# Kernel optimization log

Measured on AMD Instinct MI355X. Metric: run time of the kernel, lower is better.

## Reference

```python
import jax, jax.numpy as jnp
import numpy as np

B, V, M, C = 1024, 2, 256, 256  # batch, num_vars (must be 2), latent states, categories


def setup_inputs() -> dict:
    key = jax.random.key(0)
    k1, k2, k3 = jax.random.split(key, 3)
    x = jax.random.randint(k1, (B, V), 0, C)
    # input-node tables: per var v, per latent node k, a [M, C] row-normalized table
    W = jax.nn.softmax(jax.random.normal(k2, (V, M, M, C), dtype=jnp.float32), axis=-1)
    # sum-node mixture weights over the M product children
    w_sum = jax.nn.softmax(jax.random.normal(k3, (M,), dtype=jnp.float32))
    return {"x": x, "W": W, "w_sum": w_sum}


def reference(x, W, w_sum):
    # lp[v] has shape [M(k), M(m), B]: log W[v, k, m, x[b, v]]
    # (matches torch: probs[:, x_var].log() per input node, stacked over latent k)
    lp0 = jnp.log(W[0][:, :, x[:, 0]])  # [M, M, B]
    lp1 = jnp.log(W[1][:, :, x[:, 1]])  # [M, M, B]
    prod = lp0 + lp1                    # product nodes, [M(k), M, B]
    # sum node: log( sum_k w_k * exp(prod_k) ) -> [M, B]
    mixed = jnp.log(jnp.einsum('k,kmb->mb', w_sum, jnp.exp(prod)))
    # root: logsumexp over the leading M dim -> [B]
    return jax.nn.logsumexp(mixed, axis=0)
```

## Files before the change

kernel.cpp:

```cpp
#include <hip/hip_runtime.h>
#include <math.h>


#define SPLITS  256
#define KCHUNK  256
#define BK      32
#define NITER   (KCHUNK / BK)
#define LDSS    40

typedef float  f32x4  __attribute__((ext_vector_type(4)));
typedef short  bf16x8 __attribute__((ext_vector_type(8)));

static __device__ __forceinline__ short f2bf(float f) {
    unsigned u = __builtin_bit_cast(unsigned, f);
    u += 0x7fffu + ((u >> 16) & 1u);
    return (short)(u >> 16);
}

__global__ __launch_bounds__(512, 2) void hclt_fused_kernel(
    const int* __restrict__ x, const float* __restrict__ W,
    const float* __restrict__ wsum, float* __restrict__ S_b,
    int* __restrict__ counter, float* __restrict__ out)
{
    __shared__ __align__(16) char smem[81920];
    __shared__ int pairs[1024];
    __shared__ int lastFlag;

    short* const AsB[2] = { (short*)smem,           (short*)(smem + 20480) };
    short* const BsB[2] = { (short*)(smem + 40960), (short*)(smem + 61440) };
    float* const gat    = (float*)smem;

    const int  split = blockIdx.x;
    const long kbase = (long)split * KCHUNK;
    const float wk   = wsum[split];

    const float* __restrict__ Ag = W + kbase * 256;
    const float* __restrict__ Bg = W + 16777216 + kbase * 256;

    const int t  = threadIdx.x;
    const int cq = (t & 63) * 4;
    const int kq = (t >> 6) * 4;

    const int lane = t & 63;
    const int wv   = t >> 6;
    const int wc0  = (wv & 3) * 64;
    const int wc1  = (wv >> 2) * 128;
    const int ml   = lane & 15;
    const int qd   = lane >> 4;

    {
        const int2 x0 = ((const int2*)x)[t];
        const int2 x1 = ((const int2*)x)[t + 512];
        pairs[t]       = (x0.x << 8) | x0.y;
        pairs[t + 512] = (x1.x << 8) | x1.y;
    }

    f32x4 acc[4][8];
#pragma unroll
    for (int i = 0; i < 4; ++i)
#pragma unroll
        for (int j = 0; j < 8; ++j) acc[i][j] = (f32x4){0.f, 0.f, 0.f, 0.f};

    float4 a4[4], b4[4];

#pragma unroll
    for (int r = 0; r < 4; ++r) {
        a4[r] = *(const float4*)(Ag + (long)(kq + r) * 256 + cq);
        b4[r] = *(const float4*)(Bg + (long)(kq + r) * 256 + cq);
    }
    {
        const float* af32 = reinterpret_cast<const float*>(a4);
        const float* bf32 = reinterpret_cast<const float*>(b4);
#pragma unroll
        for (int j = 0; j < 4; ++j) {
            short4 av, bv;
            av.x = f2bf(af32[0 * 4 + j] * wk);
            av.y = f2bf(af32[1 * 4 + j] * wk);
            av.z = f2bf(af32[2 * 4 + j] * wk);
            av.w = f2bf(af32[3 * 4 + j] * wk);
            bv.x = f2bf(bf32[0 * 4 + j]);
            bv.y = f2bf(bf32[1 * 4 + j]);
            bv.z = f2bf(bf32[2 * 4 + j]);
            bv.w = f2bf(bf32[3 * 4 + j]);
            *(short4*)&AsB[0][(cq + j) * LDSS + kq] = av;
            *(short4*)&BsB[0][(cq + j) * LDSS + kq] = bv;
        }
    }
    __syncthreads();

#pragma unroll
    for (int it = 0; it < NITER; ++it) {
        const int cur = it & 1;
        if (it + 1 < NITER) {
#pragma unroll
            for (int r = 0; r < 4; ++r) {
                a4[r] = *(const float4*)(Ag + (long)((it + 1) * BK + kq + r) * 256 + cq);
                b4[r] = *(const float4*)(Bg + (long)((it + 1) * BK + kq + r) * 256 + cq);
            }
        }
        bf16x8 afr[4];
#pragma unroll
        for (int mi = 0; mi < 4; ++mi)
            afr[mi] = *(const bf16x8*)&AsB[cur][(wc0 + mi * 16 + ml) * LDSS + qd * 8];
#pragma unroll
        for (int ni = 0; ni < 8; ++ni) {
            const bf16x8 bfr = *(const bf16x8*)&BsB[cur][(wc1 + ni * 16 + ml) * LDSS + qd * 8];
#pragma unroll
            for (int mi = 0; mi < 4; ++mi)
                acc[mi][ni] = __builtin_amdgcn_mfma_f32_16x16x32_bf16(
                    afr[mi], bfr, acc[mi][ni], 0, 0, 0);
        }
        if (it + 1 < NITER) {
            const float* af32 = reinterpret_cast<const float*>(a4);
            const float* bf32 = reinterpret_cast<const float*>(b4);
#pragma unroll
            for (int j = 0; j < 4; ++j) {
                short4 av, bv;
                av.x = f2bf(af32[0 * 4 + j] * wk);
                av.y = f2bf(af32[1 * 4 + j] * wk);
                av.z = f2bf(af32[2 * 4 + j] * wk);
                av.w = f2bf(af32[3 * 4 + j] * wk);
                bv.x = f2bf(bf32[0 * 4 + j]);
                bv.y = f2bf(bf32[1 * 4 + j]);
                bv.z = f2bf(bf32[2 * 4 + j]);
                bv.w = f2bf(bf32[3 * 4 + j]);
                *(short4*)&AsB[1 - cur][(cq + j) * LDSS + kq] = av;
                *(short4*)&BsB[1 - cur][(cq + j) * LDSS + kq] = bv;
            }
            __syncthreads();
        }
    }

    const int myphase = wv >> 1, mybuf = wv & 1;
#pragma unroll 1
    for (int ph = 0; ph < 4; ++ph) {
        __syncthreads();
        if (myphase == ph) {
            float* dst = gat + mybuf * 8256;
#pragma unroll
            for (int mi = 0; mi < 4; ++mi)
#pragma unroll
                for (int ni = 0; ni < 8; ++ni)
#pragma unroll
                    for (int r = 0; r < 4; ++r)
                        dst[(mi * 16 + qd * 4 + r) * 129 + (ni * 16 + ml)] = acc[mi][ni][r];
        }
        __syncthreads();
#pragma unroll
        for (int i = t; i < 1024; i += 512) {
            const int pr = pairs[i];
            const int c0 = pr >> 8, c1 = pr & 255;
            const int own = (c0 >> 6) | ((c1 >> 7) << 2);
            if ((own >> 1) == ph) {
                const float v = gat[(own & 1) * 8256 + (c0 & 63) * 129 + (c1 & 127)];
#if defined(__gfx950__) || defined(__AMDGCN__)
                unsafeAtomicAdd(&S_b[i], v);
#else
                atomicAdd(&S_b[i], v);
#endif
            }
        }
    }

    __threadfence();
    if (t == 0) lastFlag = (atomicAdd(counter, 1) == SPLITS - 1);
    __syncthreads();
    if (lastFlag) {
        __threadfence();
#pragma unroll
        for (int i = t; i < 1024; i += 512) {
            const float s = __hip_atomic_load(&S_b[i], __ATOMIC_RELAXED,
                                              __HIP_MEMORY_SCOPE_AGENT);
            out[i] = logf(s);
        }
    }
}

extern "C" void kernel_launch(void* const* d_in, const int* in_sizes, int n_in,
                              void* d_out, int out_size, void* d_ws, size_t ws_size,
                              hipStream_t stream)
{
    const int*   x    = (const int*)d_in[0];
    const float* W    = (const float*)d_in[1];
    const float* wsum = (const float*)d_in[2];
    float* out = (float*)d_out;

    float* S_b     = (float*)d_ws;
    int*   counter = (int*)d_ws + 1024;

    hipMemsetAsync(d_ws, 0, 1024 * sizeof(float) + sizeof(int), stream);
    hclt_fused_kernel<<<dim3(SPLITS), 512, 0, stream>>>(x, W, wsum, S_b, counter, out);
}
```

Before: 247.4 us.

## Single-buffer BK=64 swizzled LDS tiles and replace atomics with two-pass reduction

Doubles the K tile to 64 and drops double buffering in favor of one swizzled LDS buffer written as 16-byte bf16x8 stores, so there are fewer barriers per chunk and fewer LDS bank conflicts. The cross-block atomic accumulation, memset and last-block counter are replaced by per-block partial writes to a workspace plus a small second kernel that sums the partials and takes the log. The gather now runs in eight single-wave phases. In exchange, the single buffer puts a barrier between compute and LDS refill, and there is an extra kernel launch and a 1 MB partials buffer.

```diff
diff --git a/kernel.cpp b/kernel.cpp
--- a/kernel.cpp
+++ b/kernel.cpp
@@ -2,11 +2,10 @@
 #include <math.h>
 
 
-#define SPLITS  256
+#define NBLK    256
 #define KCHUNK  256
-#define BK      32
+#define BK      64
 #define NITER   (KCHUNK / BK)
-#define LDSS    40
 
 typedef float  f32x4  __attribute__((ext_vector_type(4)));
 typedef short  bf16x8 __attribute__((ext_vector_type(8)));
@@ -17,43 +16,46 @@
     return (short)(u >> 16);
 }
 
-__global__ __launch_bounds__(512, 2) void hclt_fused_kernel(
+static __device__ __forceinline__ int swz(int c) {
+    return ((c >> 2) & 7) ^ ((c & 1) << 2);
+}
+
+__global__ __launch_bounds__(512, 2) void hclt_gemm(
     const int* __restrict__ x, const float* __restrict__ W,
-    const float* __restrict__ wsum, float* __restrict__ S_b,
-    int* __restrict__ counter, float* __restrict__ out)
+    const float* __restrict__ wsum, float* __restrict__ P)
 {
-    __shared__ __align__(16) char smem[81920];
+    __shared__ __align__(16) char smem[65536];
     __shared__ int pairs[1024];
-    __shared__ int lastFlag;
 
-    short* const AsB[2] = { (short*)smem,           (short*)(smem + 20480) };
-    short* const BsB[2] = { (short*)(smem + 40960), (short*)(smem + 61440) };
-    float* const gat    = (float*)smem;
+    char*  const AsB = smem;
+    char*  const BsB = smem + 32768;
+    float* const G   = (float*)smem;
 
-    const int  split = blockIdx.x;
-    const long kbase = (long)split * KCHUNK;
-    const float wk   = wsum[split];
+    const int  blk   = blockIdx.x;
+    const long kbase = (long)blk * KCHUNK;
+    const float wk   = wsum[blk];
 
     const float* __restrict__ Ag = W + kbase * 256;
     const float* __restrict__ Bg = W + 16777216 + kbase * 256;
 
-    const int t  = threadIdx.x;
-    const int cq = (t & 63) * 4;
-    const int kq = (t >> 6) * 4;
-
+    const int t    = threadIdx.x;
     const int lane = t & 63;
     const int wv   = t >> 6;
-    const int wc0  = (wv & 3) * 64;
-    const int wc1  = (wv >> 2) * 128;
-    const int ml   = lane & 15;
-    const int qd   = lane >> 4;
 
     {
-        const int2 x0 = ((const int2*)x)[t];
-        const int2 x1 = ((const int2*)x)[t + 512];
-        pairs[t]       = (x0.x << 8) | x0.y;
-        pairs[t + 512] = (x1.x << 8) | x1.y;
+        const int2 p0 = ((const int2*)x)[t];
+        const int2 p1 = ((const int2*)x)[t + 512];
+        pairs[t]       = (p0.x << 8) | p0.y;
+        pairs[t + 512] = (p1.x << 8) | p1.y;
     }
+
+    const int cq = lane * 4;
+    const int g0 = wv;
+
+    const int wc0 = (wv & 3) * 64;
+    const int wc1 = (wv >> 2) * 128;
+    const int ml  = lane & 15;
+    const int qd  = lane >> 4;
 
     f32x4 acc[4][8];
 #pragma unroll
@@ -61,119 +63,117 @@
 #pragma unroll
         for (int j = 0; j < 8; ++j) acc[i][j] = (f32x4){0.f, 0.f, 0.f, 0.f};
 
-    float4 a4[4], b4[4];
+    float4 a4[8], b4[8];
 
 #pragma unroll
-    for (int r = 0; r < 4; ++r) {
-        a4[r] = *(const float4*)(Ag + (long)(kq + r) * 256 + cq);
-        b4[r] = *(const float4*)(Bg + (long)(kq + r) * 256 + cq);
+    for (int r = 0; r < 8; ++r) {
+        a4[r] = *(const float4*)(Ag + (long)(g0 * 8 + r) * 256 + cq);
+        b4[r] = *(const float4*)(Bg + (long)(g0 * 8 + r) * 256 + cq);
     }
-    {
-        const float* af32 = reinterpret_cast<const float*>(a4);
-        const float* bf32 = reinterpret_cast<const float*>(b4);
 #pragma unroll
-        for (int j = 0; j < 4; ++j) {
-            short4 av, bv;
-            av.x = f2bf(af32[0 * 4 + j] * wk);
-            av.y = f2bf(af32[1 * 4 + j] * wk);
-            av.z = f2bf(af32[2 * 4 + j] * wk);
-            av.w = f2bf(af32[3 * 4 + j] * wk);
-            bv.x = f2bf(bf32[0 * 4 + j]);
-            bv.y = f2bf(bf32[1 * 4 + j]);
-            bv.z = f2bf(bf32[2 * 4 + j]);
-            bv.w = f2bf(bf32[3 * 4 + j]);
-            *(short4*)&AsB[0][(cq + j) * LDSS + kq] = av;
-            *(short4*)&BsB[0][(cq + j) * LDSS + kq] = bv;
+    for (int j = 0; j < 4; ++j) {
+        const int c = cq + j;
+        bf16x8 av, bv;
+#pragma unroll
+        for (int r = 0; r < 8; ++r) {
+            av[r] = f2bf(((const float*)&a4[r])[j] * wk);
+            bv[r] = f2bf(((const float*)&b4[r])[j]);
         }
+        const int off = c * 128 + (g0 ^ swz(c)) * 16;
+        *(bf16x8*)(AsB + off) = av;
+        *(bf16x8*)(BsB + off) = bv;
     }
     __syncthreads();
 
 #pragma unroll
     for (int it = 0; it < NITER; ++it) {
-        const int cur = it & 1;
         if (it + 1 < NITER) {
 #pragma unroll
-            for (int r = 0; r < 4; ++r) {
-                a4[r] = *(const float4*)(Ag + (long)((it + 1) * BK + kq + r) * 256 + cq);
-                b4[r] = *(const float4*)(Bg + (long)((it + 1) * BK + kq + r) * 256 + cq);
+            for (int r = 0; r < 8; ++r) {
+                a4[r] = *(const float4*)(Ag + (long)((it + 1) * BK + g0 * 8 + r) * 256 + cq);
+                b4[r] = *(const float4*)(Bg + (long)((it + 1) * BK + g0 * 8 + r) * 256 + cq);
             }
         }
-        bf16x8 afr[4];
 #pragma unroll
-        for (int mi = 0; mi < 4; ++mi)
-            afr[mi] = *(const bf16x8*)&AsB[cur][(wc0 + mi * 16 + ml) * LDSS + qd * 8];
+        for (int s = 0; s < 2; ++s) {
+            bf16x8 afr[4];
 #pragma unroll
-        for (int ni = 0; ni < 8; ++ni) {
-            const bf16x8 bfr = *(const bf16x8*)&BsB[cur][(wc1 + ni * 16 + ml) * LDSS + qd * 8];
+            for (int mi = 0; mi < 4; ++mi) {
+                const int c = wc0 + mi * 16 + ml;
+                afr[mi] = *(const bf16x8*)(AsB + c * 128 + (((s << 2) + qd) ^ swz(c)) * 16);
+            }
 #pragma unroll
-            for (int mi = 0; mi < 4; ++mi)
-                acc[mi][ni] = __builtin_amdgcn_mfma_f32_16x16x32_bf16(
-                    afr[mi], bfr, acc[mi][ni], 0, 0, 0);
+            for (int ni = 0; ni < 8; ++ni) {
+                const int c = wc1 + ni * 16 + ml;
+                const bf16x8 bfr =
+                    *(const bf16x8*)(BsB + c * 128 + (((s << 2) + qd) ^ swz(c)) * 16);
+#pragma unroll
+                for (int mi = 0; mi < 4; ++mi)
+                    acc[mi][ni] = __builtin_amdgcn_mfma_f32_16x16x32_bf16(
+                        afr[mi], bfr, acc[mi][ni], 0, 0, 0);
+            }
         }
         if (it + 1 < NITER) {
-            const float* af32 = reinterpret_cast<const float*>(a4);
-            const float* bf32 = reinterpret_cast<const float*>(b4);
+            __syncthreads();
 #pragma unroll
             for (int j = 0; j < 4; ++j) {
-                short4 av, bv;
-                av.x = f2bf(af32[0 * 4 + j] * wk);
-                av.y = f2bf(af32[1 * 4 + j] * wk);
-                av.z = f2bf(af32[2 * 4 + j] * wk);
-                av.w = f2bf(af32[3 * 4 + j] * wk);
-                bv.x = f2bf(bf32[0 * 4 + j]);
-                bv.y = f2bf(bf32[1 * 4 + j]);
-                bv.z = f2bf(bf32[2 * 4 + j]);
-                bv.w = f2bf(bf32[3 * 4 + j]);
-                *(short4*)&AsB[1 - cur][(cq + j) * LDSS + kq] = av;
-                *(short4*)&BsB[1 - cur][(cq + j) * LDSS + kq] = bv;
+                const int c = cq + j;
+                bf16x8 av, bv;
+#pragma unroll
+                for (int r = 0; r < 8; ++r) {
+                    av[r] = f2bf(((const float*)&a4[r])[j] * wk);
+                    bv[r] = f2bf(((const float*)&b4[r])[j]);
+                }
+                const int off = c * 128 + (g0 ^ swz(c)) * 16;
+                *(bf16x8*)(AsB + off) = av;
+                *(bf16x8*)(BsB + off) = bv;
             }
             __syncthreads();
         }
     }
 
-    const int myphase = wv >> 1, mybuf = wv & 1;
+    float v0 = 0.f, v1 = 0.f;
 #pragma unroll 1
-    for (int ph = 0; ph < 4; ++ph) {
+    for (int ph = 0; ph < 8; ++ph) {
         __syncthreads();
-        if (myphase == ph) {
-            float* dst = gat + mybuf * 8256;
+        if (wv == ph) {
 #pragma unroll
             for (int mi = 0; mi < 4; ++mi)
 #pragma unroll
                 for (int ni = 0; ni < 8; ++ni)
 #pragma unroll
                     for (int r = 0; r < 4; ++r)
-                        dst[(mi * 16 + qd * 4 + r) * 129 + (ni * 16 + ml)] = acc[mi][ni][r];
+                        G[(mi * 16 + qd * 4 + r) * 130 + (ni * 16 + ml)] = acc[mi][ni][r];
         }
         __syncthreads();
-#pragma unroll
-        for (int i = t; i < 1024; i += 512) {
-            const int pr = pairs[i];
-            const int c0 = pr >> 8, c1 = pr & 255;
-            const int own = (c0 >> 6) | ((c1 >> 7) << 2);
-            if ((own >> 1) == ph) {
-                const float v = gat[(own & 1) * 8256 + (c0 & 63) * 129 + (c1 & 127)];
-#if defined(__gfx950__) || defined(__AMDGCN__)
-                unsafeAtomicAdd(&S_b[i], v);
-#else
-                atomicAdd(&S_b[i], v);
-#endif
-            }
+        {
+            int pr = pairs[t];
+            int c0 = pr >> 8, c1 = pr & 255;
+            if ((((c0 >> 6) & 3) | ((c1 >> 7) << 2)) == ph)
+                v0 = G[(c0 & 63) * 130 + (c1 & 127)];
+            pr = pairs[t + 512];
+            c0 = pr >> 8; c1 = pr & 255;
+            if ((((c0 >> 6) & 3) | ((c1 >> 7) << 2)) == ph)
+                v1 = G[(c0 & 63) * 130 + (c1 & 127)];
         }
     }
+    P[(size_t)blk * 1024 + t]       = v0;
+    P[(size_t)blk * 1024 + 512 + t] = v1;
+}
 
-    __threadfence();
-    if (t == 0) lastFlag = (atomicAdd(counter, 1) == SPLITS - 1);
-    __syncthreads();
-    if (lastFlag) {
-        __threadfence();
-#pragma unroll
-        for (int i = t; i < 1024; i += 512) {
-            const float s = __hip_atomic_load(&S_b[i], __ATOMIC_RELAXED,
-                                              __HIP_MEMORY_SCOPE_AGENT);
-            out[i] = logf(s);
-        }
+__global__ __launch_bounds__(256) void hclt_finish(
+    const float* __restrict__ P, float* __restrict__ out)
+{
+    const int i = blockIdx.x * 256 + threadIdx.x;
+    float s0 = 0.f, s1 = 0.f, s2 = 0.f, s3 = 0.f;
+#pragma unroll 8
+    for (int s = 0; s < NBLK; s += 4) {
+        s0 += P[(size_t)(s + 0) * 1024 + i];
+        s1 += P[(size_t)(s + 1) * 1024 + i];
+        s2 += P[(size_t)(s + 2) * 1024 + i];
+        s3 += P[(size_t)(s + 3) * 1024 + i];
     }
+    out[i] = logf((s0 + s1) + (s2 + s3));
 }
 
 extern "C" void kernel_launch(void* const* d_in, const int* in_sizes, int n_in,
@@ -185,9 +185,8 @@
     const float* wsum = (const float*)d_in[2];
     float* out = (float*)d_out;
 
-    float* S_b     = (float*)d_ws;
-    int*   counter = (int*)d_ws + 1024;
+    float* P = (float*)d_ws;
 
-    hipMemsetAsync(d_ws, 0, 1024 * sizeof(float) + sizeof(int), stream);
-    hclt_fused_kernel<<<dim3(SPLITS), 512, 0, stream>>>(x, W, wsum, S_b, counter, out);
+    hclt_gemm<<<dim3(NBLK), 512, 0, stream>>>(x, W, wsum, P);
+    hclt_finish<<<dim3(4), 256, 0, stream>>>(P, out);
 }
```

New measurement: 220.3 us. -10.9%, faster.
